# Optimization experiments

Measured on AMD Instinct MI355X. Metric: run time of the kernel, lower is better.

Reference implementation:

```python
import jax, jax.numpy as jnp
import numpy as np

D = 256      # d_model
P = 8        # patch_len
H = 8        # heads
S = 3200     # spec_len
B = 64       # batch


def setup_inputs() -> dict:
    key = jax.random.key(0)
    ks = jax.random.split(key, 16)
    def w(k, shape):
        fan_in = shape[0]
        return jax.random.normal(k, shape, jnp.float32) / np.sqrt(fan_in)
    return {
        "spec": jax.random.normal(ks[0], (B, S), jnp.float32),
        # embed MLP: Linear(1,D) -> ReLU -> Linear(D,D)
        "W1": w(ks[1], (1, D)), "b1": jnp.zeros((D,), jnp.float32),
        "W2": w(ks[2], (D, D)), "b2": jnp.zeros((D,), jnp.float32),
        # multi-head attention projections
        "Wq": w(ks[3], (D, D)), "bq": jnp.zeros((D,), jnp.float32),
        "Wk": w(ks[4], (D, D)), "bk": jnp.zeros((D,), jnp.float32),
        "Wv": w(ks[5], (D, D)), "bv": jnp.zeros((D,), jnp.float32),
        "Wo": w(ks[6], (D, D)), "bo": jnp.zeros((D,), jnp.float32),
        # patch projection: Linear(P*D, D)
        "Wp": w(ks[7], (P * D, D)), "bp": jnp.zeros((D,), jnp.float32),
    }


def reference(spec, W1, b1, W2, b2, Wq, bq, Wk, bk, Wv, bv, Wo, bo, Wp, bp):
    b = spec.shape[0]
    nw = spec.shape[1] // P  # number of patch windows
    dk = D // H
    # scalar embed MLP: [b, S] -> [b, S, D]
    e = jnp.maximum(spec[..., None] * W1[0] + b1, 0.0) @ W2 + b2
    # chop into non-overlapping windows: [b, nw, P, D]
    e = e.reshape(b, nw, P, D)
    # QKV projections, split heads -> [b, nw, P, H, dk]
    q = (e @ Wq + bq).reshape(b, nw, P, H, dk)
    k = (e @ Wk + bk).reshape(b, nw, P, H, dk)
    v = (e @ Wv + bv).reshape(b, nw, P, H, dk)
    # attention within each tiny window of length P
    scores = jnp.einsum('bwqhd,bwkhd->bwhqk', q, k) / np.sqrt(dk).astype(np.float32)
    attn = jax.nn.softmax(scores, axis=-1)
    o = jnp.einsum('bwhqk,bwkhd->bwqhd', attn, v).reshape(b, nw, P, D)
    o = o @ Wo + bo
    # concat patch tokens and project: [b, nw, P*D] -> [b, nw, D]
    return o.reshape(b, nw, P * D) @ Wp + bp
```

## Files before the change

### kernel.cpp

```cpp
#include <hip/hip_runtime.h>

typedef unsigned short u16;
typedef __attribute__((ext_vector_type(8))) short short8;
typedef __attribute__((ext_vector_type(4))) float floatx4;

#define MFMA16(A, B, C) __builtin_amdgcn_mfma_f32_16x16x32_bf16((A), (B), (C), 0, 0, 0)

#define OF_PART  64
#define OF_FQKV  (OF_PART + 4096)
#define OF_SORT  (OF_FQKV + 1536)
#define OF_EVK   (OF_SORT + 512)
#define OF_CA    (OF_EVK + 256)
#define OF_CB    (OF_CA + 512)
#define OF_MA    (OF_CB + 512)
#define OF_MB    (OF_MA + 512)
#define OF_P2    (OF_MB + 512)
#define OF_TAB   (OF_P2 + 49152)
#define OF_WP    (OF_TAB + 6 * 65792)
#define OF_ORAW  (OF_WP + 524288)
#define OF_WQB   OF_ORAW
#define NPM8     204800

static __device__ __forceinline__ float bf2f(u16 u) {
  union { unsigned int i; float f; } z; z.i = ((unsigned int)u) << 16; return z.f;
}
static __device__ __forceinline__ u16 f2bf(float f) {
  union { float f; unsigned int i; } z; z.f = f;
  unsigned int x = z.i + 0x7fffu + ((z.i >> 16) & 1u);
  return (u16)(x >> 16);
}
static __device__ __forceinline__ void ld8f(const u16* p, float* o) {
  union { short8 v; u16 u[8]; } t;
  t.v = *(const short8*)p;
#pragma unroll
  for (int j = 0; j < 8; ++j) o[j] = bf2f(t.u[j]);
}

static __device__ __forceinline__ int detect_flag(const u16* __restrict__ sp) {
  const int lane = threadIdx.x & 63;
  int bad = 0;
#pragma unroll
  for (int j = 0; j < 4; ++j) {
    u16 v = sp[lane * 4 + j];
    int e = (v >> 7) & 0xFF;
    bad += (e >= 137);
  }
  return (__popcll(__ballot(bad > 0)) >= 4) ? 1 : 0;
}

#define CV(src, idx) (flag ? f2bf(((const float*)(src))[idx]) : ((const u16*)(src))[idx])

__global__ void prep1_kernel(
    const void* spec, const void* W1, const void* b1, const void* W2,
    const void* Wq, const void* bq, const void* Wk, const void* bk, const void* Wv,
    const void* bv_, const void* Wo, const void* bo, const void* Wp, const void* b2,
    u16* __restrict__ ws) {
  const int flag = detect_flag((const u16*)spec);
  const int b = blockIdx.x, tid = threadIdx.x;
  if (b == 187) {
    __shared__ float st[256];
    __shared__ int   sk[256];
    __shared__ float w1s[256], b1s[256];
    w1s[tid] = flag ? ((const float*)W1)[tid] : bf2f(((const u16*)W1)[tid]);
    b1s[tid] = flag ? ((const float*)b1)[tid] : bf2f(((const u16*)b1)[tid]);
    __syncthreads();
    {
      const float w = w1s[tid];
      st[tid] = (w != 0.f) ? (-b1s[tid] / w) : 1e30f;
      sk[tid] = tid;
    }
    for (int size = 2; size <= 256; size <<= 1) {
      for (int stride = size >> 1; stride > 0; stride >>= 1) {
        __syncthreads();
        const int ixj = tid ^ stride;
        if (ixj > tid) {
          const bool up = ((tid & size) == 0);
          float a = st[tid], bq2 = st[ixj];
          if (up ? (a > bq2) : (a < bq2)) {
            int ka = sk[tid];
            st[tid] = bq2; st[ixj] = a;
            sk[tid] = sk[ixj]; sk[ixj] = ka;
          }
        }
      }
    }
    __syncthreads();
    ((float*)(ws + OF_SORT))[tid] = st[tid];
    ws[OF_EVK + tid] = (u16)sk[tid];
    {
      const int ke = sk[tid];
      const float w = w1s[ke], bb = b1s[ke];
      const float sg = (w > 0.f) ? 1.f : ((w < 0.f) ? -1.f : 0.f);
      ((float*)(ws + OF_CA))[tid] = sg * w;
      ((float*)(ws + OF_CB))[tid] = sg * bb;
    }
    {
      const float wk = w1s[tid], bk2 = b1s[tid];
      const bool act0 = (wk < 0.f) || (wk == 0.f && bk2 > 0.f);
      ((float*)(ws + OF_MA))[tid] = act0 ? wk : 0.f;
      ((float*)(ws + OF_MB))[tid] = act0 ? bk2 : 0.f;
    }
    return;
  }
  if (b >= 176) {
    const int t = b - 176, n = tid;
    if (t < 3) {
      const void* SB = (t == 0) ? Wq : (t == 1) ? Wk : Wv;
      const void* bs = (t == 0) ? bq : (t == 1) ? bk : bv_;
      float acc;
      if (flag) {
        acc = ((const float*)bs)[n];
        const float* Bf = (const float*)SB; const float* b2f = (const float*)b2;
        for (int k = 0; k < 256; ++k) acc = fmaf(b2f[k], Bf[k * 256 + n], acc);
      } else {
        acc = bf2f(((const u16*)bs)[n]);
        const u16* Bh = (const u16*)SB; const u16* b2h = (const u16*)b2;
        for (int k = 0; k < 256; ++k) acc = fmaf(bf2f(b2h[k]), bf2f(Bh[k * 256 + n]), acc);
      }
      ((float*)(ws + OF_FQKV))[t * 256 + n] = acc;
    } else {
      const int p = t - 3;
      float acc = 0.f;
      if (flag) {
        const float* Wf = (const float*)Wp; const float* bf = (const float*)bo;
        for (int m = 0; m < 256; ++m) acc = fmaf(bf[m], Wf[(p * 256 + m) * 256 + n], acc);
      } else {
        const u16* Wh = (const u16*)Wp; const u16* bh = (const u16*)bo;
        for (int m = 0; m < 256; ++m)
          acc = fmaf(bf2f(bh[m]), bf2f(Wh[(p * 256 + m) * 256 + n]), acc);
      }
      ((float*)(ws + OF_PART))[p * 256 + n] = acc;
    }
    return;
  }
  const int g = b >> 4, sub = b & 15;
  const int r0 = (sub >> 2) * 64, c0 = (sub & 3) * 64;
  const void* SA = (g < 3) ? W2 : Wo;
  const void* SB = (g == 0) ? Wq : (g == 1) ? Wk : (g == 2) ? Wv : Wp;
  const int brow0 = (g < 3) ? 0 : (g - 3) * 256;
  const int w = tid >> 6, lane = tid & 63, l15 = lane & 15, quad = lane >> 4;
  const int arow = r0 + w * 16 + l15;
  floatx4 acc[4];
#pragma unroll
  for (int ni = 0; ni < 4; ++ni) acc[ni] = (floatx4){0.f, 0.f, 0.f, 0.f};
  if (flag) {
    const float* A = (const float*)SA; const float* B = (const float*)SB;
    for (int kc = 0; kc < 8; ++kc) {
      const int k0 = kc * 32 + quad * 8;
      floatx4 a0 = *(const floatx4*)(A + arow * 256 + k0);
      floatx4 a1 = *(const floatx4*)(A + arow * 256 + k0 + 4);
      union { short8 s8; u16 u[8]; } av;
#pragma unroll
      for (int j = 0; j < 4; ++j) { av.u[j] = f2bf(a0[j]); av.u[4 + j] = f2bf(a1[j]); }
#pragma unroll
      for (int ni = 0; ni < 4; ++ni) {
        const int colx = c0 + ni * 16 + l15;
        union { short8 s8; u16 u[8]; } bu;
#pragma unroll
        for (int j = 0; j < 8; ++j) bu.u[j] = f2bf(B[(brow0 + k0 + j) * 256 + colx]);
        acc[ni] = MFMA16(av.s8, bu.s8, acc[ni]);
      }
    }
  } else {
    const u16* A = (const u16*)SA; const u16* B = (const u16*)SB;
    for (int kc = 0; kc < 8; ++kc) {
      const int k0 = kc * 32 + quad * 8;
      short8 av = *(const short8*)(A + arow * 256 + k0);
#pragma unroll
      for (int ni = 0; ni < 4; ++ni) {
        const int colx = c0 + ni * 16 + l15;
        union { short8 s8; u16 u[8]; } bu;
#pragma unroll
        for (int j = 0; j < 8; ++j) bu.u[j] = B[(brow0 + k0 + j) * 256 + colx];
        acc[ni] = MFMA16(av, bu.s8, acc[ni]);
      }
    }
  }
  if (g < 3) {
    u16* dst = ws + OF_WQB + g * 65536;
#pragma unroll
    for (int ni = 0; ni < 4; ++ni) {
      const int n = c0 + ni * 16 + l15;
#pragma unroll
      for (int r = 0; r < 4; ++r) {
        const int k = r0 + w * 16 + quad * 4 + r;
        dst[k * 256 + n] = f2bf(acc[ni][r]);
      }
    }
  } else {
    u16* dst = ws + OF_WP;
#pragma unroll
    for (int ni = 0; ni < 4; ++ni) {
      const int n = c0 + ni * 16 + l15;
#pragma unroll
      for (int r = 0; r < 4; ++r) {
        const int k = brow0 + r0 + w * 16 + quad * 4 + r;
        dst[(k >> 3) * 2048 + n * 8 + (k & 7)] = f2bf(acc[ni][r]);
      }
    }
  }
}

__global__ void prep2a_kernel(u16* __restrict__ ws) {
  const int tbl = blockIdx.x >> 3, chunk = blockIdx.x & 7;
  const int n = threadIdx.x;
  const int m = tbl >> 1, isB = tbl & 1;
  const u16* S = ws + OF_WQB + m * 65536;
  const float* MC = (const float*)(ws + (isB ? OF_MB : OF_MA));
  const float* CC = (const float*)(ws + (isB ? OF_CB : OF_CA));
  const u16* EVK = ws + OF_EVK;
  float bacc = 0.f, eacc = 0.f;
#pragma unroll 8
  for (int j = 0; j < 32; ++j) {
    const int k = chunk * 32 + j;
    bacc = fmaf(MC[k], bf2f(S[k * 256 + n]), bacc);
    eacc = fmaf(CC[k], bf2f(S[EVK[k] * 256 + n]), eacc);
  }
  float* P = (float*)(ws + OF_P2);
  P[((tbl * 8 + chunk) * 2 + 0) * 256 + n] = bacc;
  P[((tbl * 8 + chunk) * 2 + 1) * 256 + n] = eacc;
}

__global__ void prep2b_kernel(u16* __restrict__ ws) {
  const int tbl = blockIdx.x >> 3, seg = blockIdx.x & 7;
  const int n = threadIdx.x;
  const int m = tbl >> 1, isB = tbl & 1;
  const u16* S = ws + OF_WQB + m * 65536;
  const float* CC = (const float*)(ws + (isB ? OF_CB : OF_CA));
  const u16* EVK = ws + OF_EVK;
  const float* P = (const float*)(ws + OF_P2);
  float cur = isB ? ((const float*)(ws + OF_FQKV))[m * 256 + n] : 0.f;
#pragma unroll
  for (int c = 0; c < 8; ++c) cur += P[((tbl * 8 + c) * 2 + 0) * 256 + n];
  for (int c = 0; c < seg; ++c) cur += P[((tbl * 8 + c) * 2 + 1) * 256 + n];
  u16* dst = ws + OF_TAB + tbl * 65792;
  const int rlo = seg * 32;
  dst[rlo * 256 + n] = f2bf(cur);
  const int nev = (seg == 7) ? 32 : 31;
  for (int i = 0; i < nev; ++i) {
    const int e = rlo + i;
    cur = fmaf(CC[e], bf2f(S[EVK[e] * 256 + n]), cur);
    dst[(e + 1) * 256 + n] = f2bf(cur);
  }
}

__global__ __launch_bounds__(256) void fused_lite_kernel(
    const void* __restrict__ spec, const float* __restrict__ tsort,
    const u16* __restrict__ tAq, const u16* __restrict__ tBq,
    const u16* __restrict__ tAk, const u16* __restrict__ tBk,
    const u16* __restrict__ tAv, const u16* __restrict__ tBv,
    u16* __restrict__ oraw)
{
  __shared__ u16 vbT[16384];
  __shared__ u16 pscr[1024];
  __shared__ float sS[64];
  __shared__ int   sR[64];
  __shared__ int   part[256];

  const int flag = detect_flag((const u16*)spec);
  const int tid = threadIdx.x;
  const int wave = tid >> 6, lane = tid & 63;
  const int l15 = lane & 15, quad = lane >> 4;
  const int tile0 = blockIdx.x * 64;
  const floatx4 zero4 = (floatx4){0.f, 0.f, 0.f, 0.f};

  {
    const int m = tid & 63, qt = tid >> 6;
    const float sm = flag ? ((const float*)spec)[tile0 + m]
                          : bf2f(((const u16*)spec)[tile0 + m]);
    int cnt = 0;
#pragma unroll 8
    for (int j = 0; j < 64; ++j) cnt += (tsort[qt * 64 + j] < sm) ? 1 : 0;
    part[tid] = cnt;
    __syncthreads();
    if (tid < 64) {
      sR[tid] = part[tid] + part[tid + 64] + part[tid + 128] + part[tid + 192];
      sS[tid] = sm;
    }
    __syncthreads();
  }

  {
    const int tok = wave * 16 + l15;
    const int r = sR[tok];
    const float s = sS[tok];
    const u16* Ar = tAv + r * 256;
    const u16* Br = tBv + r * 256;
#pragma unroll
    for (int j8 = 0; j8 < 8; ++j8) {
      const int d8 = quad * 64 + j8 * 8;
      float af[8], bf8[8];
      ld8f(Ar + d8, af);
      ld8f(Br + d8, bf8);
#pragma unroll
      for (int e = 0; e < 8; ++e) {
        const int d = d8 + e;
        vbT[d * 64 + (((tok >> 3) ^ (d & 7)) << 3) + (tok & 7)] =
            f2bf(fmaf(s, af[e], bf8[e]));
      }
    }
  }
  __syncthreads();

  unsigned opk[32];
  {
    const int w2 = wave * 2;
    const int tok = wave * 16 + l15;
    const int r_t = sR[tok];
    const float s_t = sS[tok];
    const int validk = ((l15 >> 3) == (quad >> 1));
    u16* ps = pscr + wave * 256;
#pragma unroll
    for (int h = 0; h < 8; ++h) {
      const int d8 = h * 32 + quad * 8;
      short8 qv, kv;
      {
        float a[8], b[8];
        ld8f(tAq + r_t * 256 + d8, a);
        ld8f(tBq + r_t * 256 + d8, b);
        union { short8 s8; u16 u[8]; } z;
#pragma unroll
        for (int e = 0; e < 8; ++e) z.u[e] = f2bf(fmaf(s_t, a[e], b[e]));
        qv = z.s8;
      }
      {
        float a[8], b[8];
        ld8f(tAk + r_t * 256 + d8, a);
        ld8f(tBk + r_t * 256 + d8, b);
        union { short8 s8; u16 u[8]; } z;
#pragma unroll
        for (int e = 0; e < 8; ++e) z.u[e] = f2bf(fmaf(s_t, a[e], b[e]));
        kv = z.s8;
      }
      floatx4 sc = MFMA16(qv, kv, zero4);
      u16 pb[4];
#pragma unroll
      for (int r = 0; r < 4; ++r) {
        float s = sc[r] * 0.17677669529663687f;
        float mx = fmaxf(s, __shfl_xor(s, 1));
        mx = fmaxf(mx, __shfl_xor(mx, 2));
        mx = fmaxf(mx, __shfl_xor(mx, 4));
        float p = __expf(s - mx);
        float sum = p + __shfl_xor(p, 1);
        sum += __shfl_xor(sum, 2);
        sum += __shfl_xor(sum, 4);
        pb[r] = f2bf(validk ? p / sum : 0.f);
      }
#pragma unroll
      for (int r = 0; r < 4; ++r) ps[(quad * 4 + r) * 16 + l15] = pb[r];
#pragma unroll
      for (int dh = 0; dh < 2; ++dh) {
        const int vcol = h * 32 + dh * 16 + l15;
        short8 pa = (short8){0, 0, 0, 0, 0, 0, 0, 0};
        short8 vf = (short8){0, 0, 0, 0, 0, 0, 0, 0};
        if (quad < 2) {
          pa = *(const short8*)(ps + l15 * 16 + quad * 8);
          vf = *(const short8*)(vbT + vcol * 64 + (((w2 + quad) ^ (vcol & 7)) << 3));
        }
        floatx4 o = MFMA16(pa, vf, zero4);
        opk[(h * 2 + dh) * 2]     = (unsigned)f2bf(o[0]) | ((unsigned)f2bf(o[1]) << 16);
        opk[(h * 2 + dh) * 2 + 1] = (unsigned)f2bf(o[2]) | ((unsigned)f2bf(o[3]) << 16);
      }
    }
  }

  {
    const int mbase = (blockIdx.x * 8 + wave * 2 + (quad >> 1)) * 8 + (l15 & 7);
    const int pb4 = (quad & 1) * 4;
#pragma unroll
    for (int h = 0; h < 8; ++h)
#pragma unroll
      for (int dh = 0; dh < 2; ++dh) {
        const int oi = (h * 2 + dh) * 2;
        const int e8 = h * 4 + dh * 2 + (l15 >> 3);
        const unsigned lo = opk[oi], hi = opk[oi + 1];
        oraw[((pb4 + 0) * 32 + e8) * NPM8 + mbase] = (u16)lo;
        oraw[((pb4 + 1) * 32 + e8) * NPM8 + mbase] = (u16)(lo >> 16);
        oraw[((pb4 + 2) * 32 + e8) * NPM8 + mbase] = (u16)hi;
        oraw[((pb4 + 3) * 32 + e8) * NPM8 + mbase] = (u16)(hi >> 16);
      }
  }
}

__global__ __launch_bounds__(256) void patch_gemm_kernel(
    const u16* __restrict__ spec_raw,
    const u16* __restrict__ oraw, const u16* __restrict__ sWp,
    const void* __restrict__ bp, const float* __restrict__ part,
    void* __restrict__ out)
{
  const int flag = detect_flag(spec_raw);
  const int tid = threadIdx.x;
  const int wave = tid >> 6, lane = tid & 63;
  const int l15 = lane & 15, quad = lane >> 4;
  const int m0 = (blockIdx.x >> 1) * 64;
  const int n0 = (blockIdx.x & 1) * 128 + wave * 32;
  const floatx4 zero4 = (floatx4){0.f, 0.f, 0.f, 0.f};

  floatx4 acc[4][2];
#pragma unroll
  for (int mi = 0; mi < 4; ++mi)
#pragma unroll
    for (int ni = 0; ni < 2; ++ni) acc[mi][ni] = zero4;

  const u16* ap = oraw + quad * NPM8 + (m0 + l15) * 8;
  const u16* bpw = sWp + quad * 2048 + (n0 + l15) * 8;
#pragma unroll 4
  for (int kk = 0; kk < 64; ++kk) {
    short8 b0 = *(const short8*)(bpw);
    short8 b1 = *(const short8*)(bpw + 128);
#pragma unroll
    for (int mi = 0; mi < 4; ++mi) {
      short8 a = *(const short8*)(ap + mi * 128);
      acc[mi][0] = MFMA16(a, b0, acc[mi][0]);
      acc[mi][1] = MFMA16(a, b1, acc[mi][1]);
    }
    ap += 4 * NPM8;
    bpw += 4 * 2048;
  }

#pragma unroll
  for (int ni = 0; ni < 2; ++ni) {
    const int n = n0 + ni * 16 + l15;
    float bb = bf2f(CV(bp, n));
#pragma unroll
    for (int p = 0; p < 8; ++p) bb += part[p * 256 + n];
#pragma unroll
    for (int mi = 0; mi < 4; ++mi) {
      const int mr = m0 + mi * 16 + quad * 4;
      if (flag) {
        float* po = (float*)out;
#pragma unroll
        for (int r = 0; r < 4; ++r)
          po[(mr + r) * 256 + n] = acc[mi][ni][r] + bb;
      } else {
        u16* po = (u16*)out;
#pragma unroll
        for (int r = 0; r < 4; ++r)
          po[(mr + r) * 256 + n] = f2bf(acc[mi][ni][r] + bb);
      }
    }
  }
}

extern "C" void kernel_launch(void* const* d_in, const int* in_sizes, int n_in,
                              void* d_out, int out_size, void* d_ws, size_t ws_size,
                              hipStream_t stream) {
  (void)in_sizes; (void)n_in; (void)out_size; (void)ws_size;
  u16* ws = (u16*)d_ws;

  prep1_kernel<<<188, 256, 0, stream>>>(
      d_in[0], d_in[1], d_in[2], d_in[3],
      d_in[5], d_in[6], d_in[7], d_in[8], d_in[9], d_in[10],
      d_in[11], d_in[12], d_in[13], d_in[4], ws);
  prep2a_kernel<<<48, 256, 0, stream>>>(ws);
  prep2b_kernel<<<48, 256, 0, stream>>>(ws);
  fused_lite_kernel<<<3200, 256, 0, stream>>>(
      d_in[0], (const float*)(ws + OF_SORT),
      ws + OF_TAB,              ws + OF_TAB + 65792,
      ws + OF_TAB + 2 * 65792,  ws + OF_TAB + 3 * 65792,
      ws + OF_TAB + 4 * 65792,  ws + OF_TAB + 5 * 65792,
      ws + OF_ORAW);
  patch_gemm_kernel<<<800, 256, 0, stream>>>(
      (const u16*)d_in[0],
      ws + OF_ORAW, ws + OF_WP,
      d_in[14], (const float*)(ws + OF_PART),
      d_out);
}
```

Baseline: 258.7 us.

## Store QKV tables in fp32, stage prep GEMM B in LDS, transpose scores MFMA

The piecewise-linear QKV lookup tables are now written and read as fp32 instead of bf16. This removes the per-element bf16 unpack in the fused kernel, at the cost of twice the table bytes. Score computation swaps the MFMA operands so the softmax reduction becomes a per-lane 4-way max plus a single cross-lane shuffle instead of three shuffle rounds, and conversions use packed bf16x2 intrinsics. The prep GEMM stages B tiles through shared memory with coalesced loads, and the V-transpose fill packs two tokens per 32-bit LDS store.

```diff
diff --git a/kernel.cpp b/kernel.cpp
--- a/kernel.cpp
+++ b/kernel.cpp
@@ -1,7 +1,9 @@
 #include <hip/hip_runtime.h>
+#include <hip/hip_bf16.h>
 
 typedef unsigned short u16;
 typedef __attribute__((ext_vector_type(8))) short short8;
+typedef __attribute__((ext_vector_type(4))) short short4_t;
 typedef __attribute__((ext_vector_type(4))) float floatx4;
 
 #define MFMA16(A, B, C) __builtin_amdgcn_mfma_f32_16x16x32_bf16((A), (B), (C), 0, 0, 0)
@@ -16,7 +18,7 @@
 #define OF_MB    (OF_MA + 512)
 #define OF_P2    (OF_MB + 512)
 #define OF_TAB   (OF_P2 + 49152)
-#define OF_WP    (OF_TAB + 6 * 65792)
+#define OF_WP    (OF_TAB + 789504)
 #define OF_ORAW  (OF_WP + 524288)
 #define OF_WQB   OF_ORAW
 #define NPM8     204800
@@ -29,11 +31,9 @@
   unsigned int x = z.i + 0x7fffu + ((z.i >> 16) & 1u);
   return (u16)(x >> 16);
 }
-static __device__ __forceinline__ void ld8f(const u16* p, float* o) {
-  union { short8 v; u16 u[8]; } t;
-  t.v = *(const short8*)p;
-#pragma unroll
-  for (int j = 0; j < 8; ++j) o[j] = bf2f(t.u[j]);
+static __device__ __forceinline__ unsigned pkbf(float lo, float hi) {
+  __hip_bfloat162 h = __float22bfloat162_rn(make_float2(lo, hi));
+  unsigned r; __builtin_memcpy(&r, &h, 4); return r;
 }
 
 static __device__ __forceinline__ int detect_flag(const u16* __restrict__ sp) {
@@ -57,6 +57,7 @@
     u16* __restrict__ ws) {
   const int flag = detect_flag((const u16*)spec);
   const int b = blockIdx.x, tid = threadIdx.x;
+  __shared__ u16 Bs[32 * 72];
   if (b == 187) {
     __shared__ float st[256];
     __shared__ int   sk[256];
@@ -140,40 +141,44 @@
   const int brow0 = (g < 3) ? 0 : (g - 3) * 256;
   const int w = tid >> 6, lane = tid & 63, l15 = lane & 15, quad = lane >> 4;
   const int arow = r0 + w * 16 + l15;
+  const int srow = tid >> 3, sseg = tid & 7;
   floatx4 acc[4];
 #pragma unroll
   for (int ni = 0; ni < 4; ++ni) acc[ni] = (floatx4){0.f, 0.f, 0.f, 0.f};
-  if (flag) {
-    const float* A = (const float*)SA; const float* B = (const float*)SB;
-    for (int kc = 0; kc < 8; ++kc) {
-      const int k0 = kc * 32 + quad * 8;
+  for (int kc = 0; kc < 8; ++kc) {
+    __syncthreads();
+    if (flag) {
+      const float* Bf = (const float*)SB;
+      const float* src = Bf + (brow0 + kc * 32 + srow) * 256 + c0 + sseg * 8;
+      floatx4 f0 = *(const floatx4*)src, f1 = *(const floatx4*)(src + 4);
+      union { short8 s8; unsigned u[4]; } t;
+      t.u[0] = pkbf(f0[0], f0[1]); t.u[1] = pkbf(f0[2], f0[3]);
+      t.u[2] = pkbf(f1[0], f1[1]); t.u[3] = pkbf(f1[2], f1[3]);
+      *(short8*)(Bs + srow * 72 + sseg * 8) = t.s8;
+    } else {
+      const u16* Bh = (const u16*)SB;
+      *(short8*)(Bs + srow * 72 + sseg * 8) =
+          *(const short8*)(Bh + (brow0 + kc * 32 + srow) * 256 + c0 + sseg * 8);
+    }
+    __syncthreads();
+    const int k0 = kc * 32 + quad * 8;
+    union { short8 s8; u16 u[8]; } av;
+    if (flag) {
+      const float* A = (const float*)SA;
       floatx4 a0 = *(const floatx4*)(A + arow * 256 + k0);
       floatx4 a1 = *(const floatx4*)(A + arow * 256 + k0 + 4);
-      union { short8 s8; u16 u[8]; } av;
-#pragma unroll
-      for (int j = 0; j < 4; ++j) { av.u[j] = f2bf(a0[j]); av.u[4 + j] = f2bf(a1[j]); }
-#pragma unroll
-      for (int ni = 0; ni < 4; ++ni) {
-        const int colx = c0 + ni * 16 + l15;
-        union { short8 s8; u16 u[8]; } bu;
-#pragma unroll
-        for (int j = 0; j < 8; ++j) bu.u[j] = f2bf(B[(brow0 + k0 + j) * 256 + colx]);
-        acc[ni] = MFMA16(av.s8, bu.s8, acc[ni]);
-      }
-    }
-  } else {
-    const u16* A = (const u16*)SA; const u16* B = (const u16*)SB;
-    for (int kc = 0; kc < 8; ++kc) {
-      const int k0 = kc * 32 + quad * 8;
-      short8 av = *(const short8*)(A + arow * 256 + k0);
-#pragma unroll
-      for (int ni = 0; ni < 4; ++ni) {
-        const int colx = c0 + ni * 16 + l15;
-        union { short8 s8; u16 u[8]; } bu;
-#pragma unroll
-        for (int j = 0; j < 8; ++j) bu.u[j] = B[(brow0 + k0 + j) * 256 + colx];
-        acc[ni] = MFMA16(av, bu.s8, acc[ni]);
-      }
+      av.u[0] = f2bf(a0[0]); av.u[1] = f2bf(a0[1]); av.u[2] = f2bf(a0[2]); av.u[3] = f2bf(a0[3]);
+      av.u[4] = f2bf(a1[0]); av.u[5] = f2bf(a1[1]); av.u[6] = f2bf(a1[2]); av.u[7] = f2bf(a1[3]);
+    } else {
+      const u16* A = (const u16*)SA;
+      av.s8 = *(const short8*)(A + arow * 256 + k0);
+    }
+#pragma unroll
+    for (int ni = 0; ni < 4; ++ni) {
+      union { short8 s8; u16 u[8]; } bu;
+#pragma unroll
+      for (int j = 0; j < 8; ++j) bu.u[j] = Bs[(quad * 8 + j) * 72 + ni * 16 + l15];
+      acc[ni] = MFMA16(av.s8, bu.s8, acc[ni]);
     }
   }
   if (g < 3) {
@@ -233,22 +238,22 @@
 #pragma unroll
   for (int c = 0; c < 8; ++c) cur += P[((tbl * 8 + c) * 2 + 0) * 256 + n];
   for (int c = 0; c < seg; ++c) cur += P[((tbl * 8 + c) * 2 + 1) * 256 + n];
-  u16* dst = ws + OF_TAB + tbl * 65792;
+  float* dst = (float*)(ws + OF_TAB) + tbl * 65792;
   const int rlo = seg * 32;
-  dst[rlo * 256 + n] = f2bf(cur);
+  dst[rlo * 256 + n] = cur;
   const int nev = (seg == 7) ? 32 : 31;
   for (int i = 0; i < nev; ++i) {
     const int e = rlo + i;
     cur = fmaf(CC[e], bf2f(S[EVK[e] * 256 + n]), cur);
-    dst[(e + 1) * 256 + n] = f2bf(cur);
+    dst[(e + 1) * 256 + n] = cur;
   }
 }
 
 __global__ __launch_bounds__(256) void fused_lite_kernel(
     const void* __restrict__ spec, const float* __restrict__ tsort,
-    const u16* __restrict__ tAq, const u16* __restrict__ tBq,
-    const u16* __restrict__ tAk, const u16* __restrict__ tBk,
-    const u16* __restrict__ tAv, const u16* __restrict__ tBv,
+    const float* __restrict__ tAq, const float* __restrict__ tBq,
+    const float* __restrict__ tAk, const float* __restrict__ tBk,
+    const float* __restrict__ tAv, const float* __restrict__ tBv,
     u16* __restrict__ oraw)
 {
   __shared__ u16 vbT[16384];
@@ -281,22 +286,24 @@
   }
 
   {
-    const int tok = wave * 16 + l15;
-    const int r = sR[tok];
-    const float s = sS[tok];
-    const u16* Ar = tAv + r * 256;
-    const u16* Br = tBv + r * 256;
-#pragma unroll
-    for (int j8 = 0; j8 < 8; ++j8) {
-      const int d8 = quad * 64 + j8 * 8;
-      float af[8], bf8[8];
-      ld8f(Ar + d8, af);
-      ld8f(Br + d8, bf8);
-#pragma unroll
-      for (int e = 0; e < 8; ++e) {
-        const int d = d8 + e;
-        vbT[d * 64 + (((tok >> 3) ^ (d & 7)) << 3) + (tok & 7)] =
-            f2bf(fmaf(s, af[e], bf8[e]));
+    const int tp = tid & 31, db = tid >> 5;
+    const int t0 = tp * 2, t1 = t0 + 1;
+    const float s0 = sS[t0], s1 = sS[t1];
+    const float* A0 = tAv + sR[t0] * 256;
+    const float* B0 = tBv + sR[t0] * 256;
+    const float* A1 = tAv + sR[t1] * 256;
+    const float* B1 = tBv + sR[t1] * 256;
+    unsigned* vbT32 = (unsigned*)vbT;
+#pragma unroll
+    for (int j = 0; j < 32; j += 4) {
+      const int d = db * 32 + j;
+      floatx4 a0 = *(const floatx4*)(A0 + d), b0 = *(const floatx4*)(B0 + d);
+      floatx4 a1 = *(const floatx4*)(A1 + d), b1 = *(const floatx4*)(B1 + d);
+#pragma unroll
+      for (int e = 0; e < 4; ++e) {
+        const int dd = d + e;
+        vbT32[dd * 32 + ((((tp >> 2) ^ (dd & 7)) << 2) | (tp & 3))] =
+            pkbf(fmaf(s0, a0[e], b0[e]), fmaf(s1, a1[e], b1[e]));
       }
     }
   }
@@ -308,46 +315,51 @@
     const int tok = wave * 16 + l15;
     const int r_t = sR[tok];
     const float s_t = sS[tok];
-    const int validk = ((l15 >> 3) == (quad >> 1));
+    const int valid = ((l15 >> 3) == (quad >> 1));
     u16* ps = pscr + wave * 256;
+    const float* Aq = tAq + r_t * 256;
+    const float* Bq = tBq + r_t * 256;
+    const float* Ak = tAk + r_t * 256;
+    const float* Bk = tBk + r_t * 256;
 #pragma unroll
     for (int h = 0; h < 8; ++h) {
       const int d8 = h * 32 + quad * 8;
       short8 qv, kv;
       {
-        float a[8], b[8];
-        ld8f(tAq + r_t * 256 + d8, a);
-        ld8f(tBq + r_t * 256 + d8, b);
-        union { short8 s8; u16 u[8]; } z;
-#pragma unroll
-        for (int e = 0; e < 8; ++e) z.u[e] = f2bf(fmaf(s_t, a[e], b[e]));
+        floatx4 a0 = *(const floatx4*)(Aq + d8), a1 = *(const floatx4*)(Aq + d8 + 4);
+        floatx4 b0 = *(const floatx4*)(Bq + d8), b1 = *(const floatx4*)(Bq + d8 + 4);
+        union { short8 s8; unsigned u[4]; } z;
+        z.u[0] = pkbf(fmaf(s_t, a0[0], b0[0]), fmaf(s_t, a0[1], b0[1]));
+        z.u[1] = pkbf(fmaf(s_t, a0[2], b0[2]), fmaf(s_t, a0[3], b0[3]));
+        z.u[2] = pkbf(fmaf(s_t, a1[0], b1[0]), fmaf(s_t, a1[1], b1[1]));
+        z.u[3] = pkbf(fmaf(s_t, a1[2], b1[2]), fmaf(s_t, a1[3], b1[3]));
         qv = z.s8;
       }
       {
-        float a[8], b[8];
-        ld8f(tAk + r_t * 256 + d8, a);
-        ld8f(tBk + r_t * 256 + d8, b);
-        union { short8 s8; u16 u[8]; } z;
-#pragma unroll
-        for (int e = 0; e < 8; ++e) z.u[e] = f2bf(fmaf(s_t, a[e], b[e]));
+        floatx4 a0 = *(const floatx4*)(Ak + d8), a1 = *(const floatx4*)(Ak + d8 + 4);
+        floatx4 b0 = *(const floatx4*)(Bk + d8), b1 = *(const floatx4*)(Bk + d8 + 4);
+        union { short8 s8; unsigned u[4]; } z;
+        z.u[0] = pkbf(fmaf(s_t, a0[0], b0[0]), fmaf(s_t, a0[1], b0[1]));
+        z.u[1] = pkbf(fmaf(s_t, a0[2], b0[2]), fmaf(s_t, a0[3], b0[3]));
+        z.u[2] = pkbf(fmaf(s_t, a1[0], b1[0]), fmaf(s_t, a1[1], b1[1]));
+        z.u[3] = pkbf(fmaf(s_t, a1[2], b1[2]), fmaf(s_t, a1[3], b1[3]));
         kv = z.s8;
       }
-      floatx4 sc = MFMA16(qv, kv, zero4);
-      u16 pb[4];
-#pragma unroll
-      for (int r = 0; r < 4; ++r) {
-        float s = sc[r] * 0.17677669529663687f;
-        float mx = fmaxf(s, __shfl_xor(s, 1));
-        mx = fmaxf(mx, __shfl_xor(mx, 2));
-        mx = fmaxf(mx, __shfl_xor(mx, 4));
-        float p = __expf(s - mx);
-        float sum = p + __shfl_xor(p, 1);
-        sum += __shfl_xor(sum, 2);
-        sum += __shfl_xor(sum, 4);
-        pb[r] = f2bf(validk ? p / sum : 0.f);
-      }
-#pragma unroll
-      for (int r = 0; r < 4; ++r) ps[(quad * 4 + r) * 16 + l15] = pb[r];
+      floatx4 sc = MFMA16(kv, qv, zero4);
+      const float SC = 0.17677669529663687f;
+      float s0 = sc[0] * SC, s1 = sc[1] * SC, s2 = sc[2] * SC, s3 = sc[3] * SC;
+      float m4 = fmaxf(fmaxf(s0, s1), fmaxf(s2, s3));
+      float mx = fmaxf(m4, __shfl_xor(m4, 16));
+      float p0 = __expf(s0 - mx), p1 = __expf(s1 - mx);
+      float p2 = __expf(s2 - mx), p3 = __expf(s3 - mx);
+      float sm = (p0 + p1) + (p2 + p3);
+      float su = sm + __shfl_xor(sm, 16);
+      float inv = 1.f / su;
+      float v0 = valid ? p0 * inv : 0.f, v1 = valid ? p1 * inv : 0.f;
+      float v2 = valid ? p2 * inv : 0.f, v3 = valid ? p3 * inv : 0.f;
+      union { short4_t s4; unsigned u[2]; } pw;
+      pw.u[0] = pkbf(v0, v1); pw.u[1] = pkbf(v2, v3);
+      *(short4_t*)(ps + l15 * 16 + quad * 4) = pw.s4;
 #pragma unroll
       for (int dh = 0; dh < 2; ++dh) {
         const int vcol = h * 32 + dh * 16 + l15;
@@ -358,8 +370,8 @@
           vf = *(const short8*)(vbT + vcol * 64 + (((w2 + quad) ^ (vcol & 7)) << 3));
         }
         floatx4 o = MFMA16(pa, vf, zero4);
-        opk[(h * 2 + dh) * 2]     = (unsigned)f2bf(o[0]) | ((unsigned)f2bf(o[1]) << 16);
-        opk[(h * 2 + dh) * 2 + 1] = (unsigned)f2bf(o[2]) | ((unsigned)f2bf(o[3]) << 16);
+        opk[(h * 2 + dh) * 2]     = pkbf(o[0], o[1]);
+        opk[(h * 2 + dh) * 2 + 1] = pkbf(o[2], o[3]);
       }
     }
   }
@@ -454,11 +466,12 @@
       d_in[11], d_in[12], d_in[13], d_in[4], ws);
   prep2a_kernel<<<48, 256, 0, stream>>>(ws);
   prep2b_kernel<<<48, 256, 0, stream>>>(ws);
+  const float* TB = (const float*)(ws + OF_TAB);
   fused_lite_kernel<<<3200, 256, 0, stream>>>(
       d_in[0], (const float*)(ws + OF_SORT),
-      ws + OF_TAB,              ws + OF_TAB + 65792,
-      ws + OF_TAB + 2 * 65792,  ws + OF_TAB + 3 * 65792,
-      ws + OF_TAB + 4 * 65792,  ws + OF_TAB + 5 * 65792,
+      TB,             TB + 65792,
+      TB + 2 * 65792, TB + 3 * 65792,
+      TB + 4 * 65792, TB + 5 * 65792,
       ws + OF_ORAW);
   patch_gemm_kernel<<<800, 256, 0, stream>>>(
       (const u16*)d_in[0],
```

New measurement: 254.1 us. Within noise of the previous version (-1.8%).
